# Performance work log

Hardware: AMD Instinct MI355X
Metric: run time of the kernel (lower is better)

The kernel has to match this reference:

```python
import jax, jax.numpy as jnp
import numpy as np

NS, NV, HE = 16, 8, 32          # scalar channels, vector (l=1) channels, edge hidden
D = NS + 3 * NV                  # flat irreps feature dim = 40
WN = NS*NS + NV*NS + NS*NV + NV*NV + NV*NV  # per-edge TP weight numel = 640
N_NODES, N_EDGES = 10000, 160000
C110 = 1.0 / np.sqrt(3.0)        # CG norm for 1o x 1o -> 0e (dot)
C111 = 1.0 / np.sqrt(2.0)        # CG norm for 1o x 1o -> 1o (cross)
EPS = 1e-5
_OFF = np.cumsum([0, NS*NS, NV*NS, NS*NV, NV*NV, NV*NV])


def _split(x):
    return x[:, :NS], x[:, NS:].reshape(x.shape[0], NV, 3)


def _flat(s, v):
    return jnp.concatenate([s, v.reshape(v.shape[0], -1)], axis=-1)


def _irreps_linear(x, Ws, Wv):
    s, v = _split(x)
    return s @ Ws, jnp.einsum('nid,io->nod', v, Wv)


def _mlp(x, w1, b1, w2, b2):
    return jax.nn.relu(x @ w1 + b1) @ w2 + b2


def _tp(x_s, x_v, sh, w):
    # equivariant tensor product (feat 16x0e+8x1o) x (sh 1x0e+1x1o) -> (16x0e+8x1o)
    E = x_s.shape[0]
    sh_s, sh_v = sh[:, 0], sh[:, 1:4]
    w1 = w[:, _OFF[0]:_OFF[1]].reshape(E, NS, NS)  # 0e x 0e -> 0e
    w2 = w[:, _OFF[1]:_OFF[2]].reshape(E, NV, NS)  # 1o x 1o -> 0e (dot)
    w3 = w[:, _OFF[2]:_OFF[3]].reshape(E, NS, NV)  # 0e x 1o -> 1o
    w4 = w[:, _OFF[3]:_OFF[4]].reshape(E, NV, NV)  # 1o x 0e -> 1o
    w5 = w[:, _OFF[4]:_OFF[5]].reshape(E, NV, NV)  # 1o x 1o -> 1o (cross)
    dot = jnp.einsum('eid,ed->ei', x_v, sh_v)
    cross = jnp.cross(x_v, sh_v[:, None, :])
    out_s = (jnp.einsum('eio,ei->eo', w1, x_s * sh_s[:, None])
             + C110 * jnp.einsum('eio,ei->eo', w2, dot))
    out_v = (jnp.einsum('eio,ei,ed->eod', w3, x_s, sh_v)
             + jnp.einsum('eio,eid->eod', w4, x_v * sh_s[:, None, None])
             + C111 * jnp.einsum('eio,eid->eod', w5, cross))
    return out_s, out_v


def _batchnorm(x, w_s, b_s, w_v):
    # e3nn-style BatchNorm: standard BN on scalars, norm-normalization on vectors
    s, v = _split(x)
    mu, var = s.mean(0), s.var(0)
    s = (s - mu) / jnp.sqrt(var + EPS) * w_s + b_s
    norm = (v * v).mean(-1).mean(0)  # [NV]
    v = v / jnp.sqrt(norm + EPS)[None, :, None] * w_v[None, :, None]
    return _flat(s, v)


def setup_inputs() -> dict:
    key = jax.random.key(0)
    ks = jax.random.split(key, 12)
    g = lambda i, shape, sc=1.0: jax.random.normal(ks[i], shape, jnp.float32) * sc
    return {
        'atom_features': g(0, (N_NODES, D)),
        'edge_features': g(1, (N_EDGES, HE)),
        'edge_sh': g(2, (N_EDGES, 4)),
        'Wq_s': g(3, (NS, NS), 1.0 / np.sqrt(NS)),
        'Wq_v': g(4, (NV, NV), 1.0 / np.sqrt(NV)),
        'k_w1': g(5, (HE, HE), 1.0 / np.sqrt(HE)), 'k_b1': jnp.zeros((HE,), jnp.float32),
        'k_w2': g(6, (HE, WN), 1.0 / np.sqrt(HE)), 'k_b2': jnp.zeros((WN,), jnp.float32),
        'v_w1': g(7, (HE, HE), 1.0 / np.sqrt(HE)), 'v_b1': jnp.zeros((HE,), jnp.float32),
        'v_w2': g(8, (HE, WN), 1.0 / np.sqrt(HE)), 'v_b2': jnp.zeros((WN,), jnp.float32),
        'bn_w_s': jnp.ones((NS,), jnp.float32), 'bn_b_s': jnp.zeros((NS,), jnp.float32),
        'bn_w_v': jnp.ones((NV,), jnp.float32),
        'edge_index': jax.random.randint(ks[9], (2, N_EDGES), 0, N_NODES),
    }


def reference(atom_features, edge_features, edge_sh, Wq_s, Wq_v,
              k_w1, k_b1, k_w2, k_b2, v_w1, v_b1, v_w2, v_b2,
              bn_w_s, bn_b_s, bn_w_v, edge_index):
    edge_dst, edge_src = edge_index[0], edge_index[1]
    q = _flat(*_irreps_linear(atom_features, Wq_s, Wq_v))[edge_src]     # [E, D]
    x_s, x_v = _split(atom_features[edge_dst])
    k = _flat(*_tp(x_s, x_v, edge_sh, _mlp(edge_features, k_w1, k_b1, k_w2, k_b2)))
    v = _flat(*_tp(x_s, x_v, edge_sh, _mlp(edge_features, v_w1, v_b1, v_w2, v_b2)))
    attn = jnp.sum(q * k, axis=-1)                                       # [E]
    m = jax.ops.segment_max(attn, edge_src, num_segments=N_NODES)
    m = jnp.where(jnp.isfinite(m), m, 0.0)
    e = jnp.exp(attn - m[edge_src])
    denom = jax.ops.segment_sum(e, edge_src, num_segments=N_NODES)
    a = e / denom[edge_src]
    upd = jax.ops.segment_sum(v * a[:, None], edge_src, num_segments=N_NODES)
    out = _batchnorm(atom_features + upd, bn_w_s, bn_b_s, bn_w_v)
    return out, edge_features
```

## Files before the change

### kernel.cpp

```cpp
#include <hip/hip_runtime.h>
#include <hip/hip_bf16.h>

typedef unsigned short u16;
typedef unsigned int u32;
typedef _Float16 h16;

#define NNODES 10000
#define NEDGES 160000

#define C110 0.57735026918962576f
#define C111 0.70710678118654752f

typedef __attribute__((ext_vector_type(8))) _Float16 half8;
typedef __attribute__((ext_vector_type(4))) float f32x4;

__device__ int   g_isf32;
__device__ float g_q[NNODES * 40];
__device__ float g_x[NNODES * 40];
__device__ float g_attn[NEDGES];
__device__ float g_stats64[64][40];
__device__ u16   g_vb16[(size_t)NEDGES * 40];
__device__ u32   g_m8[8 * NNODES];
__device__ u32   g_cnt8[8 * NNODES];
__device__ int   g_bucket[(size_t)NNODES * 128];
__device__ h16   g_w1hk[1024], g_w1lk[1024], g_w1hv[1024], g_w1lv[1024];
__device__ __align__(16) h16 g_w2k[640 * 32];
__device__ __align__(16) h16 g_w2v[640 * 32];
__device__ float g_b1k[32], g_b1v[32], g_b2k[640], g_b2v[640];

__device__ __forceinline__ float bf2f(u16 v) {
    return __uint_as_float(((u32)v) << 16);
}
__device__ __forceinline__ u32 f2bfbits(float f) {
    u32 u = __float_as_uint(f);
    u32 r = 0x7FFFu + ((u >> 16) & 1u);
    return (u + r) >> 16;
}
__device__ __forceinline__ u32 pack2(float a, float b) {
    return f2bfbits(a) | (f2bfbits(b) << 16);
}
__device__ __forceinline__ u32 encf(float f) {
    u32 u = __float_as_uint(f);
    return (u & 0x80000000u) ? ~u : (u | 0x80000000u);
}
__device__ __forceinline__ float decf(u32 u) {
    return (u & 0x80000000u) ? __uint_as_float(u & 0x7FFFFFFFu) : __uint_as_float(~u);
}
__device__ __forceinline__ float ldx(const void* p, size_t i, int f32) {
    return f32 ? ((const float*)p)[i] : bf2f(((const u16*)p)[i]);
}
__device__ __forceinline__ void split2h(float v, h16& hi, h16& lo) {
    h16 h = (h16)v;
    hi = h;
    lo = (h16)(v - (float)h);
}
__device__ __forceinline__ void unp8(uint4 v, float* x) {
    x[0] = bf2f((u16)(v.x & 0xffffu)); x[1] = bf2f((u16)(v.x >> 16));
    x[2] = bf2f((u16)(v.y & 0xffffu)); x[3] = bf2f((u16)(v.y >> 16));
    x[4] = bf2f((u16)(v.z & 0xffffu)); x[5] = bf2f((u16)(v.z >> 16));
    x[6] = bf2f((u16)(v.w & 0xffffu)); x[7] = bf2f((u16)(v.w >> 16));
}
__device__ __forceinline__ void gld16(const void* g, void* l) {
    __builtin_amdgcn_global_load_lds(
        (__attribute__((address_space(1))) void*)(uintptr_t)g,
        (__attribute__((address_space(3))) void*)l, 16, 0, 0);
}

__global__ __launch_bounds__(256) void k_pre(
    const void* __restrict__ atom, const void* __restrict__ Wqs,
    const void* __restrict__ Wqv,
    const void* __restrict__ kw1, const void* __restrict__ kb1,
    const void* __restrict__ kw2, const void* __restrict__ kb2,
    const void* __restrict__ vw1, const void* __restrict__ vb1,
    const void* __restrict__ vw2, const void* __restrict__ vb2,
    const void* __restrict__ ef, void* __restrict__ out) {
    __shared__ int sF32;
    __shared__ float sW[320];
    const int tid = threadIdx.x;
    const u16* atom16 = (const u16*)atom;

    if (tid < 64) {
        int cnt = 0;
        #pragma unroll 4
        for (int j = tid * 16; j < tid * 16 + 16; ++j) {
            float ve = bf2f(atom16[2 * j]);
            float ae = fabsf(ve);
            if (ve == 0.f || (ae > 9.3e-13f && ae < 1.1e12f)) cnt++;
        }
        cnt += __shfl_xor(cnt, 1);  cnt += __shfl_xor(cnt, 2);
        cnt += __shfl_xor(cnt, 4);  cnt += __shfl_xor(cnt, 8);
        cnt += __shfl_xor(cnt, 16); cnt += __shfl_xor(cnt, 32);
        if (tid == 0) {
            int r = (cnt < 716) ? 1 : 0;
            sF32 = r;
            if (blockIdx.x == 0) g_isf32 = r;
        }
    }
    __syncthreads();
    const int f32 = sF32;

    int i = blockIdx.x * 256 + tid;
    if (i < 8 * NNODES) {
        g_cnt8[i] = 0u;
        g_m8[i] = 0x007FFFFFu;
    }
    if (i < 64 * 40) ((float*)g_stats64)[i] = 0.f;

    if (blockIdx.x >= 40 && blockIdx.x < 120) {
        int t = i - 10240;
        if (t < 640 * 32) {
            int k = t / 640, n = t - k * 640;
            g_w2k[n * 32 + k] = (h16)ldx(kw2, t, f32);
            g_w2v[n * 32 + k] = (h16)ldx(vw2, t, f32);
        }
        if (t < 1024) {
            int s = t >> 5, tt = t & 31;
            split2h(ldx(kw1, t, f32), g_w1hk[tt * 32 + s], g_w1lk[tt * 32 + s]);
            split2h(ldx(vw1, t, f32), g_w1hv[tt * 32 + s], g_w1lv[tt * 32 + s]);
        }
        if (t < 640) { g_b2k[t] = ldx(kb2, t, f32); g_b2v[t] = ldx(vb2, t, f32); }
        if (t < 32)  { g_b1k[t] = ldx(kb1, t, f32); g_b1v[t] = ldx(vb1, t, f32); }
    } else if (blockIdx.x < 40) {
        sW[tid] = ldx(Wqs, tid, f32);
        if (tid < 64) sW[256 + tid] = ldx(Wqv, tid, f32);
        __syncthreads();
        int n = i;
        if (n >= NNODES) return;
        float x[40];
        if (f32) {
            const float4* ap = (const float4*)((const float*)atom + (size_t)n * 40);
            #pragma unroll
            for (int c = 0; c < 10; ++c) {
                float4 v = ap[c];
                x[c*4+0] = v.x; x[c*4+1] = v.y; x[c*4+2] = v.z; x[c*4+3] = v.w;
            }
        } else {
            const uint4* ap = (const uint4*)((const u16*)atom + (size_t)n * 40);
            #pragma unroll
            for (int c = 0; c < 5; ++c) unp8(ap[c], x + c * 8);
        }
        float qs[16];
        #pragma unroll
        for (int o = 0; o < 16; ++o) qs[o] = 0.f;
        #pragma unroll 1
        for (int ii = 0; ii < 16; ++ii) {
            float ai = x[ii];
            #pragma unroll
            for (int o = 0; o < 16; ++o) qs[o] = fmaf(ai, sW[ii * 16 + o], qs[o]);
        }
        float qv[24];
        #pragma unroll
        for (int k = 0; k < 24; ++k) qv[k] = 0.f;
        #pragma unroll 1
        for (int ii = 0; ii < 8; ++ii) {
            float a0 = x[16 + 3*ii + 0], a1 = x[16 + 3*ii + 1], a2 = x[16 + 3*ii + 2];
            #pragma unroll
            for (int o = 0; o < 8; ++o) {
                float wv = sW[256 + ii * 8 + o];
                qv[o*3+0] = fmaf(a0, wv, qv[o*3+0]);
                qv[o*3+1] = fmaf(a1, wv, qv[o*3+1]);
                qv[o*3+2] = fmaf(a2, wv, qv[o*3+2]);
            }
        }
        float* qp = g_q + (size_t)n * 40;
        #pragma unroll
        for (int o = 0; o < 16; ++o) qp[o] = qs[o];
        #pragma unroll
        for (int k = 0; k < 24; ++k) qp[16 + k] = qv[k];
    } else {
        const size_t b = blockIdx.x - 120;
        if (f32) {
            const uint4* s = (const uint4*)ef;
            uint4* d = (uint4*)((char*)out + 1600000u);
            for (size_t idx = b * 256 + tid; idx < 1280000u; idx += 200u * 256u)
                d[idx] = s[idx];
        } else {
            const uint4* s = (const uint4*)ef;
            uint4* d = (uint4*)((char*)out + 800000u);
            for (size_t idx = b * 256 + tid; idx < 640000u; idx += 200u * 256u)
                d[idx] = s[idx];
        }
    }
}

#define ACCS 41

#define STAGE(cc, WK, WV) do { \
    gld16((const char*)g_w2k + (cc)*4096 + w*1024 + lane*16, (char*)(WK) + w*1024); \
    gld16((const char*)g_w2v + (cc)*4096 + w*1024 + lane*16, (char*)(WV) + w*1024); \
} while (0)

#define TILE(nt, WK, WV) do { \
    const int tl_ = (nt) & 3; \
    half8 bk = *(const half8*)((WK) + (tl_*16 + c) * 32 + quad * 8); \
    half8 bv = *(const half8*)((WV) + (tl_*16 + c) * 32 + quad * 8); \
    float bbk = sB2k[(nt)*16 + c], bbv = sB2v[(nt)*16 + c]; \
    f32x4 Ck = {0.f,0.f,0.f,0.f}, Cv = {0.f,0.f,0.f,0.f}; \
    Ck = __builtin_amdgcn_mfma_f32_16x16x32_f16(aflk, bk, Ck, 0, 0, 0); \
    Ck = __builtin_amdgcn_mfma_f32_16x16x32_f16(afhk, bk, Ck, 0, 0, 0); \
    Cv = __builtin_amdgcn_mfma_f32_16x16x32_f16(aflv, bv, Cv, 0, 0, 0); \
    Cv = __builtin_amdgcn_mfma_f32_16x16x32_f16(afhv, bv, Cv, 0, 0, 0); \
    if ((nt) < 16) { \
        f32x4 xf = *(const f32x4*)(smF + (8 + (nt)) * 64 + e0); \
        _Pragma("unroll") \
        for (int r = 0; r < 4; ++r) { float fr = xf[r] * ssf[r]; \
            aSk[r] = fmaf(Ck[r] + bbk, fr, aSk[r]); \
            aSv[r] = fmaf(Cv[r] + bbv, fr, aSv[r]); } \
    } else if ((nt) < 24) { \
        f32x4 f = *(const f32x4*)(smF + ((nt) - 16) * 64 + e0); \
        _Pragma("unroll") \
        for (int r = 0; r < 4; ++r) { \
            aSk[r] = fmaf(Ck[r] + bbk, f[r], aSk[r]); \
            aSv[r] = fmaf(Cv[r] + bbv, f[r], aSv[r]); } \
    } else if ((nt) < 32) { \
        f32x4 f = *(const f32x4*)(smF + (8 + 2*((nt)-24) + ch) * 64 + e0); \
        _Pragma("unroll") \
        for (int r = 0; r < 4; ++r) { \
            aTk[r] = fmaf(Ck[r] + bbk, f[r], aTk[r]); \
            aTv[r] = fmaf(Cv[r] + bbv, f[r], aTv[r]); } \
    } else if ((nt) < 36) { \
        const int i_ = 2*((nt)-32) + ch; \
        _Pragma("unroll") \
        for (int d = 0; d < 3; ++d) { \
            f32x4 f = *(const f32x4*)(smF + (24 + d*8 + i_) * 64 + e0); \
            _Pragma("unroll") \
            for (int r = 0; r < 4; ++r) { \
                aVk[d*4+r] = fmaf(Ck[r] + bbk, f[r], aVk[d*4+r]); \
                aVv[d*4+r] = fmaf(Cv[r] + bbv, f[r], aVv[d*4+r]); } } \
    } else { \
        const int i_ = 2*((nt)-36) + ch; \
        _Pragma("unroll") \
        for (int d = 0; d < 3; ++d) { \
            f32x4 f = *(const f32x4*)(smF + (48 + d*8 + i_) * 64 + e0); \
            _Pragma("unroll") \
            for (int r = 0; r < 4; ++r) { \
                aVk[d*4+r] = fmaf(Ck[r] + bbk, f[r], aVk[d*4+r]); \
                aVv[d*4+r] = fmaf(Cv[r] + bbv, f[r], aVv[d*4+r]); } } \
    } \
} while (0)

#define DO_CHUNK(cc, WK, WV) do { \
    TILE((cc)*4 + 0, WK, WV); \
    TILE((cc)*4 + 1, WK, WV); \
    TILE((cc)*4 + 2, WK, WV); \
    TILE((cc)*4 + 3, WK, WV); \
} while (0)

__global__ __launch_bounds__(256, 4) void k_edge(
    const void* __restrict__ atom, const void* __restrict__ ef,
    const void* __restrict__ sh, const int* __restrict__ ei,
    void* __restrict__ out) {
    __shared__ __align__(16) float smF[76 * 64];
    __shared__ __align__(16) h16 sWkA[2048], sWvA[2048];
    __shared__ __align__(16) h16 sWkB[2048], sWvB[2048];
    __shared__ float sB2k[640], sB2v[640];

    const int f32 = g_isf32;
    const int t = threadIdx.x;
    const int w = t >> 6, lane = t & 63;
    const int quad = lane >> 4, c = lane & 15;
    const int eb = blockIdx.x * 64;
    const int slice = blockIdx.x & 7;

    STAGE(0, sWkA, sWvA);
    for (int i2 = t; i2 < 640; i2 += 256) { sB2k[i2] = g_b2k[i2]; sB2v[i2] = g_b2v[i2]; }

    half8 efh, efl;
    {
        const size_t base = (size_t)(eb + w * 16 + c) * 32 + quad * 8;
        h16 th, tl;
        if (f32) {
            const float4* ep = (const float4*)((const float*)ef + base);
            float4 v0 = ep[0], v1 = ep[1];
            split2h(v0.x, th, tl); efh[0] = th; efl[0] = tl;
            split2h(v0.y, th, tl); efh[1] = th; efl[1] = tl;
            split2h(v0.z, th, tl); efh[2] = th; efl[2] = tl;
            split2h(v0.w, th, tl); efh[3] = th; efl[3] = tl;
            split2h(v1.x, th, tl); efh[4] = th; efl[4] = tl;
            split2h(v1.y, th, tl); efh[5] = th; efl[5] = tl;
            split2h(v1.z, th, tl); efh[6] = th; efl[6] = tl;
            split2h(v1.w, th, tl); efh[7] = th; efl[7] = tl;
        } else {
            uint4 v = *(const uint4*)((const u16*)ef + base);
            float xe[8];
            unp8(v, xe);
            #pragma unroll
            for (int j = 0; j < 8; ++j) {
                split2h(xe[j], th, tl);
                efh[j] = th; efl[j] = tl;
            }
        }
    }

    if (lane < 16) {
        const int e = w * 16 + lane;
        const int ge = eb + e;
        const int dst = ei[ge];
        float x[40];
        float ss, s0, s1, s2;
        if (f32) {
            const float4* xp = (const float4*)((const float*)atom + (size_t)dst * 40);
            #pragma unroll
            for (int i = 0; i < 10; ++i) {
                float4 v = xp[i];
                x[i*4+0] = v.x; x[i*4+1] = v.y; x[i*4+2] = v.z; x[i*4+3] = v.w;
            }
            float4 s4 = *(const float4*)((const float*)sh + (size_t)ge * 4);
            ss = s4.x; s0 = s4.y; s1 = s4.z; s2 = s4.w;
        } else {
            const uint4* xp = (const uint4*)((const u16*)atom + (size_t)dst * 40);
            #pragma unroll
            for (int i = 0; i < 5; ++i) unp8(xp[i], x + i * 8);
            uint2 s2v = *(const uint2*)((const u16*)sh + (size_t)ge * 4);
            ss = bf2f((u16)(s2v.x & 0xffffu)); s0 = bf2f((u16)(s2v.x >> 16));
            s1 = bf2f((u16)(s2v.y & 0xffffu)); s2 = bf2f((u16)(s2v.y >> 16));
        }
        #pragma unroll
        for (int i = 0; i < 16; ++i)
            smF[(8 + i) * 64 + e] = x[i];
        #pragma unroll
        for (int i = 0; i < 8; ++i) {
            float a0 = x[16+3*i], a1 = x[17+3*i], a2 = x[18+3*i];
            smF[i * 64 + e]        = C110 * (a0*s0 + a1*s1 + a2*s2);
            smF[(24 + i) * 64 + e] = a0 * ss;
            smF[(32 + i) * 64 + e] = a1 * ss;
            smF[(40 + i) * 64 + e] = a2 * ss;
            smF[(48 + i) * 64 + e] = C111 * (a1*s2 - a2*s1);
            smF[(56 + i) * 64 + e] = C111 * (a2*s0 - a0*s2);
            smF[(64 + i) * 64 + e] = C111 * (a0*s1 - a1*s0);
        }
        smF[72*64 + e] = s0; smF[73*64 + e] = s1; smF[74*64 + e] = s2;
        smF[75*64 + e] = ss;
    }

    half8 afhk, aflk, afhv, aflv;
    #pragma unroll
    for (int p = 0; p < 2; ++p) {
        const h16* w1h = p ? g_w1hv : g_w1hk;
        const h16* w1l = p ? g_w1lv : g_w1lk;
        const float* b1 = p ? g_b1v : g_b1k;
        f32x4 H0, H1;
        #pragma unroll
        for (int nt = 0; nt < 2; ++nt) {
            half8 ah = *(const half8*)(w1h + (nt*16 + c) * 32 + quad * 8);
            half8 al = *(const half8*)(w1l + (nt*16 + c) * 32 + quad * 8);
            f32x4 D = {0.f, 0.f, 0.f, 0.f};
            D = __builtin_amdgcn_mfma_f32_16x16x32_f16(al, efh, D, 0, 0, 0);
            D = __builtin_amdgcn_mfma_f32_16x16x32_f16(ah, efl, D, 0, 0, 0);
            D = __builtin_amdgcn_mfma_f32_16x16x32_f16(ah, efh, D, 0, 0, 0);
            #pragma unroll
            for (int r = 0; r < 4; ++r)
                D[r] = fmaxf(D[r] + b1[nt*16 + quad*4 + r], 0.f);
            if (nt == 0) H0 = D; else H1 = D;
        }
        half8 th8, tl8;
        #pragma unroll
        for (int j = 0; j < 8; ++j) {
            int sl = (((2*quad + (j >> 2)) & 3) << 4) + c;
            float v0 = __shfl(H0[j & 3], sl);
            float v1 = __shfl(H1[j & 3], sl);
            float val = (quad < 2) ? v0 : v1;
            h16 hh, ll;
            split2h(val, hh, ll);
            th8[j] = hh; tl8[j] = ll;
        }
        if (p == 0) { afhk = th8; aflk = tl8; }
        else        { afhv = th8; aflv = tl8; }
    }

    const int e0 = w * 16 + quad * 4;
    const int o = c & 7, ch = c >> 3;

    f32x4 ssf = *(const f32x4*)(smF + 75*64 + e0);

    float aSk[4] = {0.f,0.f,0.f,0.f}, aTk[4] = {0.f,0.f,0.f,0.f};
    float aVk[12] = {0.f,0.f,0.f,0.f,0.f,0.f,0.f,0.f,0.f,0.f,0.f,0.f};
    float aSv[4] = {0.f,0.f,0.f,0.f}, aTv[4] = {0.f,0.f,0.f,0.f};
    float aVv[12] = {0.f,0.f,0.f,0.f,0.f,0.f,0.f,0.f,0.f,0.f,0.f,0.f};

    __syncthreads();
    STAGE(1, sWkB, sWvB);  DO_CHUNK(0, sWkA, sWvA);
    __syncthreads();
    STAGE(2, sWkA, sWvA);  DO_CHUNK(1, sWkB, sWvB);
    __syncthreads();
    STAGE(3, sWkB, sWvB);  DO_CHUNK(2, sWkA, sWvA);
    __syncthreads();
    STAGE(4, sWkA, sWvA);  DO_CHUNK(3, sWkB, sWvB);
    __syncthreads();
    STAGE(5, sWkB, sWvB);  DO_CHUNK(4, sWkA, sWvA);
    __syncthreads();
    STAGE(6, sWkA, sWvA);  DO_CHUNK(5, sWkB, sWvB);
    __syncthreads();
    STAGE(7, sWkB, sWvB);  DO_CHUNK(6, sWkA, sWvA);
    __syncthreads();
    STAGE(8, sWkA, sWvA);  DO_CHUNK(7, sWkB, sWvB);
    __syncthreads();
    STAGE(9, sWkB, sWvB);  DO_CHUNK(8, sWkA, sWvA);
    __syncthreads();
    DO_CHUNK(9, sWkB, sWvB);
    __syncthreads();

    float* const accp = smF + w * 656;

    const int el = lane >> 2, part = lane & 3;
    const int ge2 = eb + w * 16 + el;

    #pragma unroll
    for (int r = 0; r < 4; ++r) accp[(quad*4 + r) * ACCS + c] = aSk[r];
    #pragma unroll
    for (int r = 0; r < 4; ++r) aTk[r] += __shfl_xor(aTk[r], 8);
    #pragma unroll
    for (int d = 0; d < 3; ++d)
        #pragma unroll
        for (int r = 0; r < 4; ++r) aVk[d*4+r] += __shfl_xor(aVk[d*4+r], 8);
    if (ch == 0) {
        #pragma unroll
        for (int d = 0; d < 3; ++d) {
            f32x4 sv = *(const f32x4*)(smF + (72 + d) * 64 + e0);
            #pragma unroll
            for (int r = 0; r < 4; ++r)
                accp[(quad*4 + r) * ACCS + 16 + o*3 + d] = aVk[d*4+r] + aTk[r] * sv[r];
        }
    }
    {
        const int src = ei[NEDGES + ge2];
        const float* qp = g_q + (size_t)src * 40 + part * 10;
        const float* ap = accp + el * ACCS + part * 10;
        float partial = 0.f;
        #pragma unroll
        for (int d2 = 0; d2 < 10; ++d2) partial = fmaf(qp[d2], ap[d2], partial);
        partial += __shfl_xor(partial, 1);
        partial += __shfl_xor(partial, 2);
        if (part == 0) {
            g_attn[ge2] = partial;
            atomicMax(&g_m8[slice * NNODES + src], encf(partial));
            u32 pos = atomicAdd(&g_cnt8[slice * NNODES + src], 1u);
            if (pos < 16u) g_bucket[(size_t)src * 128 + slice * 16 + pos] = ge2;
        }
    }

    #pragma unroll
    for (int r = 0; r < 4; ++r) accp[(quad*4 + r) * ACCS + c] = aSv[r];
    #pragma unroll
    for (int r = 0; r < 4; ++r) aTv[r] += __shfl_xor(aTv[r], 8);
    #pragma unroll
    for (int d = 0; d < 3; ++d)
        #pragma unroll
        for (int r = 0; r < 4; ++r) aVv[d*4+r] += __shfl_xor(aVv[d*4+r], 8);
    if (ch == 0) {
        #pragma unroll
        for (int d = 0; d < 3; ++d) {
            f32x4 sv = *(const f32x4*)(smF + (72 + d) * 64 + e0);
            #pragma unroll
            for (int r = 0; r < 4; ++r)
                accp[(quad*4 + r) * ACCS + 16 + o*3 + d] = aVv[d*4+r] + aTv[r] * sv[r];
        }
    }
    {
        u32* vb = (u32*)(g_vb16 + (size_t)ge2 * 40) + part * 5;
        const float* ap = accp + el * ACCS + part * 10;
        #pragma unroll
        for (int d2 = 0; d2 < 5; ++d2) vb[d2] = pack2(ap[2*d2], ap[2*d2+1]);
    }
}

__global__ __launch_bounds__(256) void k_post(const void* __restrict__ atom) {
    __shared__ float part_s[40];
    __shared__ int   sse[4][128];
    __shared__ float ssp[4][128];
    const int f32 = g_isf32;
    const int w = threadIdx.x >> 6;
    const int node = blockIdx.x * 4 + w;
    const int lane = threadIdx.x & 63;
    if (threadIdx.x < 40) part_s[threadIdx.x] = 0.f;
    __syncthreads();

    float m = -__builtin_huge_valf();
    #pragma unroll
    for (int s = 0; s < 8; ++s) m = fmaxf(m, decf(g_m8[s * NNODES + node]));

    float p0 = 0.f, p1 = 0.f;
    int eA = 0, eB = 0;
    {
        const int idx = lane & 15;
        u32 c0 = g_cnt8[(lane >> 4) * NNODES + node];
        if (c0 > 16u) c0 = 16u;
        if ((u32)idx < c0) {
            eA = g_bucket[(size_t)node * 128 + lane];
            p0 = expf(fminf(g_attn[eA] - m, 0.f));
        }
        u32 c1 = g_cnt8[(4 + (lane >> 4)) * NNODES + node];
        if (c1 > 16u) c1 = 16u;
        if ((u32)idx < c1) {
            eB = g_bucket[(size_t)node * 128 + 64 + lane];
            p1 = expf(fminf(g_attn[eB] - m, 0.f));
        }
    }
    float dv = p0 + p1;
    dv += __shfl_xor(dv, 1);  dv += __shfl_xor(dv, 2);
    dv += __shfl_xor(dv, 4);  dv += __shfl_xor(dv, 8);
    dv += __shfl_xor(dv, 16); dv += __shfl_xor(dv, 32);
    const float den = dv;

    const unsigned long long below = (1ull << lane) - 1ull;
    unsigned long long mk0 = __ballot(p0 != 0.f);
    if (p0 != 0.f) {
        int idx = (int)__popcll(mk0 & below);
        sse[w][idx] = eA; ssp[w][idx] = p0;
    }
    int n0 = (int)__popcll(mk0);
    unsigned long long mk1 = __ballot(p1 != 0.f);
    if (p1 != 0.f) {
        int idx = n0 + (int)__popcll(mk1 & below);
        sse[w][idx] = eB; ssp[w][idx] = p1;
    }
    const int n = n0 + (int)__popcll(mk1);

    float a0 = 0.f, a1 = 0.f, a2 = 0.f, a3 = 0.f;
    if (lane < 40) {
        int k = 0;
        for (; k + 4 <= n; k += 4) {
            a0 = fmaf(ssp[w][k+0], bf2f(g_vb16[(size_t)sse[w][k+0] * 40 + lane]), a0);
            a1 = fmaf(ssp[w][k+1], bf2f(g_vb16[(size_t)sse[w][k+1] * 40 + lane]), a1);
            a2 = fmaf(ssp[w][k+2], bf2f(g_vb16[(size_t)sse[w][k+2] * 40 + lane]), a2);
            a3 = fmaf(ssp[w][k+3], bf2f(g_vb16[(size_t)sse[w][k+3] * 40 + lane]), a3);
        }
        for (; k < n; ++k)
            a0 = fmaf(ssp[w][k], bf2f(g_vb16[(size_t)sse[w][k] * 40 + lane]), a0);
    }
    float acc = (a0 + a1) + (a2 + a3);

    float inv = (den > 0.f) ? 1.f / den : 0.f;
    float xv = 0.f;
    if (lane < 40) {
        xv = ldx(atom, (size_t)node * 40 + lane, f32) + acc * inv;
        g_x[(size_t)node * 40 + lane] = xv;
    }
    if (lane < 16) {
        atomicAdd(&part_s[lane], xv);
        atomicAdd(&part_s[16 + lane], xv * xv);
    }
    float sq = xv * xv;
    float tri = sq + __shfl_down(sq, 1) + __shfl_down(sq, 2);
    if (lane >= 16 && lane < 40 && ((lane - 16) % 3 == 0))
        atomicAdd(&part_s[32 + (lane - 16) / 3], tri);
    __syncthreads();
    if (threadIdx.x < 40)
        atomicAdd(&g_stats64[blockIdx.x & 63][threadIdx.x], part_s[threadIdx.x]);
}

__global__ __launch_bounds__(256) void k_out(
    const void* __restrict__ bws, const void* __restrict__ bbs,
    const void* __restrict__ bwv, void* __restrict__ out) {
    __shared__ float sst[40];
    __shared__ float spar[40];
    const int f32 = g_isf32;
    int t = threadIdx.x;
    const float invN = 1.f / (float)NNODES;
    if (t < 40) {
        float s_ = 0.f;
        #pragma unroll 8
        for (int s = 0; s < 64; ++s) s_ += g_stats64[s][t];
        sst[t] = s_;
    }
    __syncthreads();
    if (t < 16) {
        float mu = sst[t] * invN;
        float var = fmaxf(sst[16 + t] * invN - mu * mu, 0.f);
        float isd = 1.f / sqrtf(var + 1e-5f);
        float sc = ldx(bws, t, f32) * isd;
        spar[t] = sc;
        spar[16 + t] = ldx(bbs, t, f32) - mu * sc;
    } else if (t >= 32 && t < 40) {
        int i = t - 32;
        float norm = sst[t] * (invN / 3.f);
        spar[t] = ldx(bwv, i, f32) / sqrtf(norm + 1e-5f);
    }
    __syncthreads();

    int n = blockIdx.x * 256 + t;
    if (n >= NNODES) return;
    const float4* xp4 = (const float4*)(g_x + (size_t)n * 40);
    float xp[40];
    #pragma unroll
    for (int c = 0; c < 10; ++c) {
        float4 v = xp4[c];
        xp[c*4+0] = v.x; xp[c*4+1] = v.y; xp[c*4+2] = v.z; xp[c*4+3] = v.w;
    }
    float res[40];
    #pragma unroll
    for (int c = 0; c < 16; ++c) res[c] = xp[c] * spar[c] + spar[16 + c];
    #pragma unroll
    for (int i = 0; i < 8; ++i) {
        float s = spar[32 + i];
        res[16+3*i+0] = xp[16+3*i+0] * s;
        res[16+3*i+1] = xp[16+3*i+1] * s;
        res[16+3*i+2] = xp[16+3*i+2] * s;
    }
    if (f32) {
        float4* op = (float4*)((float*)out + (size_t)n * 40);
        #pragma unroll
        for (int c = 0; c < 10; ++c)
            op[c] = make_float4(res[c*4+0], res[c*4+1], res[c*4+2], res[c*4+3]);
    } else {
        uint4* op = (uint4*)((u16*)out + (size_t)n * 40);
        #pragma unroll
        for (int c = 0; c < 5; ++c) {
            uint4 r;
            r.x = pack2(res[c*8+0], res[c*8+1]);
            r.y = pack2(res[c*8+2], res[c*8+3]);
            r.z = pack2(res[c*8+4], res[c*8+5]);
            r.w = pack2(res[c*8+6], res[c*8+7]);
            op[c] = r;
        }
    }
}

extern "C" void kernel_launch(void* const* d_in, const int* in_sizes, int n_in,
                              void* d_out, int out_size, void* d_ws, size_t ws_size,
                              hipStream_t stream) {
    const void* atom = d_in[0];
    const void* ef   = d_in[1];
    const void* sh   = d_in[2];
    const void* Wqs  = d_in[3];
    const void* Wqv  = d_in[4];
    const void* kw1  = d_in[5];
    const void* kb1  = d_in[6];
    const void* kw2  = d_in[7];
    const void* kb2  = d_in[8];
    const void* vw1  = d_in[9];
    const void* vb1  = d_in[10];
    const void* vw2  = d_in[11];
    const void* vb2  = d_in[12];
    const void* bws  = d_in[13];
    const void* bbs  = d_in[14];
    const void* bwv  = d_in[15];
    const int*  ei   = (const int*)d_in[16];

    k_pre <<<320, 256, 0, stream>>>(atom, Wqs, Wqv, kw1, kb1, kw2, kb2,
                                    vw1, vb1, vw2, vb2, ef, d_out);
    k_edge<<<2500, 256, 0, stream>>>(atom, ef, sh, ei, d_out);
    k_post<<<2500, 256, 0, stream>>>(atom);
    k_out <<<40, 256, 0, stream>>>(bws, bbs, bwv, d_out);
}
```

Before: 189.2 us.

## Store attention scores in edge buckets and compute segment max in post

The edge kernel now writes each edge's attention score next to its edge id in an int2 bucket entry. This replaces the separate g_attn array and the per-slice atomicMax into encoded max buffers. The post kernel takes the segment max with a wave shuffle reduction over the bucket scores, which removes the edge-indexed gather of attention values and the max atomics. The MFMA accumulators are also seeded with the bias instead of adding it per element, and the weighted gather loop is unrolled to 8 accumulators. The trade-off is a larger bucket store, and the bias now enters the accumulator before the split hi/lo products.

Result: no change. 189.5 us (+0.2%).

```diff
diff --git a/kernel.cpp b/kernel.cpp
--- a/kernel.cpp
+++ b/kernel.cpp
@@ -17,12 +17,10 @@
 __device__ int   g_isf32;
 __device__ float g_q[NNODES * 40];
 __device__ float g_x[NNODES * 40];
-__device__ float g_attn[NEDGES];
 __device__ float g_stats64[64][40];
 __device__ u16   g_vb16[(size_t)NEDGES * 40];
-__device__ u32   g_m8[8 * NNODES];
 __device__ u32   g_cnt8[8 * NNODES];
-__device__ int   g_bucket[(size_t)NNODES * 128];
+__device__ int2  g_bucket2[(size_t)NNODES * 128];
 __device__ h16   g_w1hk[1024], g_w1lk[1024], g_w1hv[1024], g_w1lv[1024];
 __device__ __align__(16) h16 g_w2k[640 * 32];
 __device__ __align__(16) h16 g_w2v[640 * 32];
@@ -38,13 +36,6 @@
 }
 __device__ __forceinline__ u32 pack2(float a, float b) {
     return f2bfbits(a) | (f2bfbits(b) << 16);
-}
-__device__ __forceinline__ u32 encf(float f) {
-    u32 u = __float_as_uint(f);
-    return (u & 0x80000000u) ? ~u : (u | 0x80000000u);
-}
-__device__ __forceinline__ float decf(u32 u) {
-    return (u & 0x80000000u) ? __uint_as_float(u & 0x7FFFFFFFu) : __uint_as_float(~u);
 }
 __device__ __forceinline__ float ldx(const void* p, size_t i, int f32) {
     return f32 ? ((const float*)p)[i] : bf2f(((const u16*)p)[i]);
@@ -100,10 +91,7 @@
     const int f32 = sF32;
 
     int i = blockIdx.x * 256 + tid;
-    if (i < 8 * NNODES) {
-        g_cnt8[i] = 0u;
-        g_m8[i] = 0x007FFFFFu;
-    }
+    if (i < 8 * NNODES) g_cnt8[i] = 0u;
     if (i < 64 * 40) ((float*)g_stats64)[i] = 0.f;
 
     if (blockIdx.x >= 40 && blockIdx.x < 120) {
@@ -195,7 +183,8 @@
     half8 bk = *(const half8*)((WK) + (tl_*16 + c) * 32 + quad * 8); \
     half8 bv = *(const half8*)((WV) + (tl_*16 + c) * 32 + quad * 8); \
     float bbk = sB2k[(nt)*16 + c], bbv = sB2v[(nt)*16 + c]; \
-    f32x4 Ck = {0.f,0.f,0.f,0.f}, Cv = {0.f,0.f,0.f,0.f}; \
+    f32x4 Ck = {bbk, bbk, bbk, bbk}; \
+    f32x4 Cv = {bbv, bbv, bbv, bbv}; \
     Ck = __builtin_amdgcn_mfma_f32_16x16x32_f16(aflk, bk, Ck, 0, 0, 0); \
     Ck = __builtin_amdgcn_mfma_f32_16x16x32_f16(afhk, bk, Ck, 0, 0, 0); \
     Cv = __builtin_amdgcn_mfma_f32_16x16x32_f16(aflv, bv, Cv, 0, 0, 0); \
@@ -204,20 +193,20 @@
         f32x4 xf = *(const f32x4*)(smF + (8 + (nt)) * 64 + e0); \
         _Pragma("unroll") \
         for (int r = 0; r < 4; ++r) { float fr = xf[r] * ssf[r]; \
-            aSk[r] = fmaf(Ck[r] + bbk, fr, aSk[r]); \
-            aSv[r] = fmaf(Cv[r] + bbv, fr, aSv[r]); } \
+            aSk[r] = fmaf(Ck[r], fr, aSk[r]); \
+            aSv[r] = fmaf(Cv[r], fr, aSv[r]); } \
     } else if ((nt) < 24) { \
         f32x4 f = *(const f32x4*)(smF + ((nt) - 16) * 64 + e0); \
         _Pragma("unroll") \
         for (int r = 0; r < 4; ++r) { \
-            aSk[r] = fmaf(Ck[r] + bbk, f[r], aSk[r]); \
-            aSv[r] = fmaf(Cv[r] + bbv, f[r], aSv[r]); } \
+            aSk[r] = fmaf(Ck[r], f[r], aSk[r]); \
+            aSv[r] = fmaf(Cv[r], f[r], aSv[r]); } \
     } else if ((nt) < 32) { \
         f32x4 f = *(const f32x4*)(smF + (8 + 2*((nt)-24) + ch) * 64 + e0); \
         _Pragma("unroll") \
         for (int r = 0; r < 4; ++r) { \
-            aTk[r] = fmaf(Ck[r] + bbk, f[r], aTk[r]); \
-            aTv[r] = fmaf(Cv[r] + bbv, f[r], aTv[r]); } \
+            aTk[r] = fmaf(Ck[r], f[r], aTk[r]); \
+            aTv[r] = fmaf(Cv[r], f[r], aTv[r]); } \
     } else if ((nt) < 36) { \
         const int i_ = 2*((nt)-32) + ch; \
         _Pragma("unroll") \
@@ -225,8 +214,8 @@
             f32x4 f = *(const f32x4*)(smF + (24 + d*8 + i_) * 64 + e0); \
             _Pragma("unroll") \
             for (int r = 0; r < 4; ++r) { \
-                aVk[d*4+r] = fmaf(Ck[r] + bbk, f[r], aVk[d*4+r]); \
-                aVv[d*4+r] = fmaf(Cv[r] + bbv, f[r], aVv[d*4+r]); } } \
+                aVk[d*4+r] = fmaf(Ck[r], f[r], aVk[d*4+r]); \
+                aVv[d*4+r] = fmaf(Cv[r], f[r], aVv[d*4+r]); } } \
     } else { \
         const int i_ = 2*((nt)-36) + ch; \
         _Pragma("unroll") \
@@ -234,8 +223,8 @@
             f32x4 f = *(const f32x4*)(smF + (48 + d*8 + i_) * 64 + e0); \
             _Pragma("unroll") \
             for (int r = 0; r < 4; ++r) { \
-                aVk[d*4+r] = fmaf(Ck[r] + bbk, f[r], aVk[d*4+r]); \
-                aVv[d*4+r] = fmaf(Cv[r] + bbv, f[r], aVv[d*4+r]); } } \
+                aVk[d*4+r] = fmaf(Ck[r], f[r], aVk[d*4+r]); \
+                aVv[d*4+r] = fmaf(Cv[r], f[r], aVv[d*4+r]); } } \
     } \
 } while (0)
 
@@ -432,10 +421,13 @@
         partial += __shfl_xor(partial, 1);
         partial += __shfl_xor(partial, 2);
         if (part == 0) {
-            g_attn[ge2] = partial;
-            atomicMax(&g_m8[slice * NNODES + src], encf(partial));
             u32 pos = atomicAdd(&g_cnt8[slice * NNODES + src], 1u);
-            if (pos < 16u) g_bucket[(size_t)src * 128 + slice * 16 + pos] = ge2;
+            if (pos < 16u) {
+                int2 ent;
+                ent.x = ge2;
+                ent.y = __float_as_int(partial);
+                g_bucket2[(size_t)src * 128 + slice * 16 + pos] = ent;
+            }
         }
     }
 
@@ -475,27 +467,26 @@
     if (threadIdx.x < 40) part_s[threadIdx.x] = 0.f;
     __syncthreads();
 
-    float m = -__builtin_huge_valf();
-    #pragma unroll
-    for (int s = 0; s < 8; ++s) m = fmaxf(m, decf(g_m8[s * NNODES + node]));
-
-    float p0 = 0.f, p1 = 0.f;
-    int eA = 0, eB = 0;
-    {
-        const int idx = lane & 15;
-        u32 c0 = g_cnt8[(lane >> 4) * NNODES + node];
-        if (c0 > 16u) c0 = 16u;
-        if ((u32)idx < c0) {
-            eA = g_bucket[(size_t)node * 128 + lane];
-            p0 = expf(fminf(g_attn[eA] - m, 0.f));
-        }
-        u32 c1 = g_cnt8[(4 + (lane >> 4)) * NNODES + node];
-        if (c1 > 16u) c1 = 16u;
-        if ((u32)idx < c1) {
-            eB = g_bucket[(size_t)node * 128 + 64 + lane];
-            p1 = expf(fminf(g_attn[eB] - m, 0.f));
-        }
-    }
+    const int idx = lane & 15;
+    u32 c0 = g_cnt8[(lane >> 4) * NNODES + node];
+    u32 c1 = g_cnt8[(4 + (lane >> 4)) * NNODES + node];
+    int2 b0 = g_bucket2[(size_t)node * 128 + lane];
+    int2 b1 = g_bucket2[(size_t)node * 128 + 64 + lane];
+    if (c0 > 16u) c0 = 16u;
+    if (c1 > 16u) c1 = 16u;
+    const bool v0 = (u32)idx < c0, v1 = (u32)idx < c1;
+
+    const float NEGINF = -__builtin_huge_valf();
+    float a0v = v0 ? __int_as_float(b0.y) : NEGINF;
+    float a1v = v1 ? __int_as_float(b1.y) : NEGINF;
+    float m = fmaxf(a0v, a1v);
+    m = fmaxf(m, __shfl_xor(m, 1));  m = fmaxf(m, __shfl_xor(m, 2));
+    m = fmaxf(m, __shfl_xor(m, 4));  m = fmaxf(m, __shfl_xor(m, 8));
+    m = fmaxf(m, __shfl_xor(m, 16)); m = fmaxf(m, __shfl_xor(m, 32));
+
+    float p0 = v0 ? expf(a0v - m) : 0.f;
+    float p1 = v1 ? expf(a1v - m) : 0.f;
+
     float dv = p0 + p1;
     dv += __shfl_xor(dv, 1);  dv += __shfl_xor(dv, 2);
     dv += __shfl_xor(dv, 4);  dv += __shfl_xor(dv, 8);
@@ -505,30 +496,39 @@
     const unsigned long long below = (1ull << lane) - 1ull;
     unsigned long long mk0 = __ballot(p0 != 0.f);
     if (p0 != 0.f) {
-        int idx = (int)__popcll(mk0 & below);
-        sse[w][idx] = eA; ssp[w][idx] = p0;
+        int cidx = (int)__popcll(mk0 & below);
+        sse[w][cidx] = b0.x; ssp[w][cidx] = p0;
     }
     int n0 = (int)__popcll(mk0);
     unsigned long long mk1 = __ballot(p1 != 0.f);
     if (p1 != 0.f) {
-        int idx = n0 + (int)__popcll(mk1 & below);
-        sse[w][idx] = eB; ssp[w][idx] = p1;
+        int cidx = n0 + (int)__popcll(mk1 & below);
+        sse[w][cidx] = b1.x; ssp[w][cidx] = p1;
     }
     const int n = n0 + (int)__popcll(mk1);
 
     float a0 = 0.f, a1 = 0.f, a2 = 0.f, a3 = 0.f;
+    float a4 = 0.f, a5 = 0.f, a6 = 0.f, a7 = 0.f;
     if (lane < 40) {
         int k = 0;
-        for (; k + 4 <= n; k += 4) {
+        for (; k + 8 <= n; k += 8) {
             a0 = fmaf(ssp[w][k+0], bf2f(g_vb16[(size_t)sse[w][k+0] * 40 + lane]), a0);
             a1 = fmaf(ssp[w][k+1], bf2f(g_vb16[(size_t)sse[w][k+1] * 40 + lane]), a1);
             a2 = fmaf(ssp[w][k+2], bf2f(g_vb16[(size_t)sse[w][k+2] * 40 + lane]), a2);
             a3 = fmaf(ssp[w][k+3], bf2f(g_vb16[(size_t)sse[w][k+3] * 40 + lane]), a3);
-        }
-        for (; k < n; ++k)
+            a4 = fmaf(ssp[w][k+4], bf2f(g_vb16[(size_t)sse[w][k+4] * 40 + lane]), a4);
+            a5 = fmaf(ssp[w][k+5], bf2f(g_vb16[(size_t)sse[w][k+5] * 40 + lane]), a5);
+            a6 = fmaf(ssp[w][k+6], bf2f(g_vb16[(size_t)sse[w][k+6] * 40 + lane]), a6);
+            a7 = fmaf(ssp[w][k+7], bf2f(g_vb16[(size_t)sse[w][k+7] * 40 + lane]), a7);
+        }
+        for (; k + 2 <= n; k += 2) {
+            a0 = fmaf(ssp[w][k+0], bf2f(g_vb16[(size_t)sse[w][k+0] * 40 + lane]), a0);
+            a1 = fmaf(ssp[w][k+1], bf2f(g_vb16[(size_t)sse[w][k+1] * 40 + lane]), a1);
+        }
+        if (k < n)
             a0 = fmaf(ssp[w][k], bf2f(g_vb16[(size_t)sse[w][k] * 40 + lane]), a0);
     }
-    float acc = (a0 + a1) + (a2 + a3);
+    float acc = ((a0 + a1) + (a2 + a3)) + ((a4 + a5) + (a6 + a7));
 
     float inv = (den > 0.f) ? 1.f / den : 0.f;
     float xv = 0.f;
```
